# Kernel tuning notes

Hardware: AMD Instinct MI355X
Metric: run time of the kernel (lower is better)

## Reference

```python
import jax, jax.numpy as jnp
import numpy as np

H = 4  # head_num = 8 // 2
NEG = -1e9


def mha(x, mask, wqkv, bqkv, wo, bo):
    # x: [B, N, D], mask: [B, 1, N] (0 = masked key), wqkv: [3, D, D], wo: [D, Dout]
    B, N, D = x.shape
    dh = D // H
    q = (x @ wqkv[0] + bqkv[0]).reshape(B, N, H, dh)
    k = (x @ wqkv[1] + bqkv[1]).reshape(B, N, H, dh)
    v = (x @ wqkv[2] + bqkv[2]).reshape(B, N, H, dh)
    scores = jnp.einsum('bqhd,bkhd->bhqk', q, k) / jnp.sqrt(jnp.asarray(dh, x.dtype))
    scores = jnp.where(mask[:, None, :, :] == 0, NEG, scores)  # mask keys, bcast over heads/queries
    attn = jax.nn.softmax(scores, axis=-1)
    out = jnp.einsum('bhqk,bkhd->bqhd', attn, v).reshape(B, N, D)
    return out @ wo + bo


def setup_inputs() -> dict:
    key = jax.random.key(0)
    ks = jax.random.split(key, 24)
    B, M, F = 16, 32, 16
    N = M * M
    def w(k, shape, fan_in):
        return jax.random.normal(k, shape, dtype=jnp.float32) / np.sqrt(fan_in)
    return {
        'robot_1_node': jax.random.normal(ks[0], (B, M, F), dtype=jnp.float32),
        'robot_2_node': jax.random.normal(ks[1], (B, M, F), dtype=jnp.float32),
        'coop_edge_cost': jax.random.normal(ks[2], (B, M, M, F), dtype=jnp.float32),
        'coop_edge_mask': jax.random.randint(ks[3], (B, M, M), 0, 2, dtype=jnp.int32),
        'd1_wqkv': w(ks[4], (3, 48, 48), 48), 'd1_bqkv': jnp.zeros((3, 48), jnp.float32),
        'd1_wo': w(ks[5], (48, 16), 48), 'd1_bo': jnp.zeros((16,), jnp.float32),
        'd2_wqkv': w(ks[6], (3, 16, 16), 16), 'd2_bqkv': jnp.zeros((3, 16), jnp.float32),
        'd2_wo': w(ks[7], (16, 16), 16), 'd2_bo': jnp.zeros((16,), jnp.float32),
        'pol_wqkv': w(ks[8], (3, 16, 16), 16), 'pol_bqkv': jnp.zeros((3, 16), jnp.float32),
        'pol_wo': w(ks[9], (16, 1), 16), 'pol_bo': jnp.zeros((1,), jnp.float32),
        'val_wqkv': w(ks[10], (3, 16, 16), 16), 'val_bqkv': jnp.zeros((3, 16), jnp.float32),
        'val_wo': w(ks[11], (16, 1), 16), 'val_bo': jnp.zeros((1,), jnp.float32),
        'v2_w': w(ks[12], (N, 16), N), 'v2_b': jnp.zeros((16,), jnp.float32),
    }


def reference(robot_1_node, robot_2_node, coop_edge_cost, coop_edge_mask,
              d1_wqkv, d1_bqkv, d1_wo, d1_bo,
              d2_wqkv, d2_bqkv, d2_wo, d2_bo,
              pol_wqkv, pol_bqkv, pol_wo, pol_bo,
              val_wqkv, val_bqkv, val_wo, val_bo,
              v2_w, v2_b):
    B, M, F = robot_1_node.shape
    N = M * M
    edge = coop_edge_cost.reshape(B, N, -1)            # flatten(-3,-2)
    mask = coop_edge_mask.reshape(B, 1, N)             # flatten + unsqueeze(-2)
    f1 = jnp.broadcast_to(robot_1_node[:, :, None, :], (B, M, M, F)).reshape(B, N, F)
    f2 = jnp.broadcast_to(robot_2_node[:, None, :, :], (B, M, M, F)).reshape(B, N, F)
    f = jnp.concatenate([f1, f2, edge], axis=-1)       # [B, N, 3F]
    e = mha(f, mask, d1_wqkv, d1_bqkv, d1_wo, d1_bo)   # [B, N, 16]
    e = mha(e, mask, d2_wqkv, d2_bqkv, d2_wo, d2_bo)   # [B, N, 16]
    action = mha(e, mask, pol_wqkv, pol_bqkv, pol_wo, pol_bo).reshape(B, N)
    masked_action = jax.nn.softmax(jnp.where(mask[:, 0, :] == 0, NEG, action), axis=-1)
    critic = mha(e, mask, val_wqkv, val_bqkv, val_wo, val_bo).reshape(B, N)
    critic = critic @ v2_w + v2_b                       # [B, 16]
    return masked_action, critic
```

## Files before the change

kernel.cpp:

```cpp
#include <hip/hip_runtime.h>
#include <math.h>

#define NEGV (-1e9f)
#define LOG2E 1.4426950408889634f

typedef _Float16 f16;
typedef __attribute__((ext_vector_type(2))) __fp16 hf2;
typedef __attribute__((ext_vector_type(4))) _Float16 f16x4;
typedef __attribute__((ext_vector_type(4))) float f32x4;

__global__ void qkv1_prep_kernel(
    const float* __restrict__ r1, const float* __restrict__ r2,
    const float* __restrict__ edge,
    const float* __restrict__ d1_wqkv, const float* __restrict__ d1_bqkv,
    const float* __restrict__ d1_wo, const float* __restrict__ d1_bo,
    const float* __restrict__ d2_wqkv, const float* __restrict__ d2_bqkv,
    const float* __restrict__ d2_wo, const float* __restrict__ d2_bo,
    const float* __restrict__ pol_wqkv, const float* __restrict__ pol_bqkv,
    const float* __restrict__ val_wqkv, const float* __restrict__ val_bqkv,
    f16* __restrict__ q1h, f16* __restrict__ k1h, f16* __restrict__ v1h,
    float* __restrict__ Wf1, float* __restrict__ bf1,
    float* __restrict__ Wfp, float* __restrict__ bfp,
    float* __restrict__ Wfv, float* __restrict__ bfv,
    int B, int M, int F, int H, float qmul1, int mainBlocks) {
    const int N = M * M;
    const int BN = B * N;

    if ((int)blockIdx.x < mainBlocks) {
        int t = blockIdx.x * blockDim.x + threadIdx.x;
        if (t >= 3 * BN * 48) return;
        int col = t % 48;
        int row = (t / 48) % BN;
        int mat = t / (48 * BN);
        int b = row / N, n = row % N;
        int i = n / M, j = n % M;

        const float* f1 = r1 + (b * M + i) * F;
        const float* f2 = r2 + (b * M + j) * F;
        const float* fe = edge + (size_t)row * F;
        const float* w  = d1_wqkv + mat * 48 * 48 + col;

        float s = d1_bqkv[mat * 48 + col];
#pragma unroll
        for (int d = 0; d < 16; ++d) s = fmaf(f1[d], w[d * 48], s);
#pragma unroll
        for (int d = 0; d < 16; ++d) s = fmaf(f2[d], w[(16 + d) * 48], s);
#pragma unroll
        for (int d = 0; d < 16; ++d) s = fmaf(fe[d], w[(32 + d) * 48], s);

        int h = col / 12, dd = col % 12;
        size_t off = ((size_t)(b * H + h) * N + n) * 12 + dd;
        if (mat == 0)      q1h[off] = (f16)(s * qmul1);
        else if (mat == 1) k1h[off] = (f16)s;
        else               v1h[off] = (f16)s;
        return;
    }

    int t = (blockIdx.x - mainBlocks) * 256 + threadIdx.x;
    if (t < 2304) {
        int mat = t / 768, r = (t % 768) / 16, c = t % 16;
        float s = 0.f;
#pragma unroll
        for (int k = 0; k < 16; ++k)
            s = fmaf(d1_wo[r * 16 + k], d2_wqkv[mat * 256 + k * 16 + c], s);
        Wf1[t] = s;
        return;
    }
    int u = t - 2304;
    if (u < 48) {
        int mat = u / 16, c = u % 16;
        float s = d2_bqkv[mat * 16 + c];
#pragma unroll
        for (int k = 0; k < 16; ++k)
            s = fmaf(d1_bo[k], d2_wqkv[mat * 256 + k * 16 + c], s);
        bf1[u] = s;
        return;
    }
    u -= 48;
    if (u < 768) {
        int mat = u / 256, r = (u % 256) / 16, c = u % 16;
        float s = 0.f;
#pragma unroll
        for (int k = 0; k < 16; ++k)
            s = fmaf(d2_wo[r * 16 + k], pol_wqkv[mat * 256 + k * 16 + c], s);
        Wfp[u] = s;
        return;
    }
    u -= 768;
    if (u < 48) {
        int mat = u / 16, c = u % 16;
        float s = pol_bqkv[mat * 16 + c];
#pragma unroll
        for (int k = 0; k < 16; ++k)
            s = fmaf(d2_bo[k], pol_wqkv[mat * 256 + k * 16 + c], s);
        bfp[u] = s;
        return;
    }
    u -= 48;
    if (u < 768) {
        int mat = u / 256, r = (u % 256) / 16, c = u % 16;
        float s = 0.f;
#pragma unroll
        for (int k = 0; k < 16; ++k)
            s = fmaf(d2_wo[r * 16 + k], val_wqkv[mat * 256 + k * 16 + c], s);
        Wfv[u] = s;
        return;
    }
    u -= 768;
    if (u < 48) {
        int mat = u / 16, c = u % 16;
        float s = val_bqkv[mat * 16 + c];
#pragma unroll
        for (int k = 0; k < 16; ++k)
            s = fmaf(d2_bo[k], val_wqkv[mat * 256 + k * 16 + c], s);
        bfv[u] = s;
    }
}

template <int DH>
__device__ inline void attn_core(const f16* __restrict__ qh, const f16* __restrict__ kh,
                                 const f16* __restrict__ vh, const int* __restrict__ mask,
                                 int b, int qg, int H, int N,
                                 f16* __restrict__ Kt, f16* __restrict__ Vt,
                                 float* __restrict__ mbs,
                                 float* __restrict__ comb, int combStride) {
    int tid = threadIdx.x;
    int wave = tid >> 6, lane = tid & 63;
    int h = wave & 3, qhalf = wave >> 2;
    int lrow = lane & 15, lg = lane >> 4;
    int bhs = b * H + h;
    int qrow = qg * 32 + qhalf * 16 + lrow;

    f16x4 zf = {(f16)0.f, (f16)0.f, (f16)0.f, (f16)0.f};
    bool qok = (4 * lg < DH);
    f16x4 qf = qok ? *(const f16x4*)(qh + ((size_t)bhs * N + qrow) * DH + 4 * lg) : zf;

    f32x4 oacc = {0.f, 0.f, 0.f, 0.f};

    for (int chunk = 0; chunk < 4; ++chunk) {
        int kbase = chunk * 256;
        __syncthreads();
        for (int idx = tid; idx < 1024; idx += 512) {
            int hh = idx >> 8, kk = idx & 255;
            const f16* kB = kh + ((size_t)(b * H + hh) * N + kbase + kk) * DH;
            const f16* vB = vh + ((size_t)(b * H + hh) * N + kbase + kk) * DH;
#pragma unroll
            for (int d4 = 0; d4 < DH / 4; ++d4)
                ((uint2*)(Kt + ((size_t)hh * 256 + kk) * DH))[d4] = ((const uint2*)kB)[d4];
            uint2 vr[DH / 4];
#pragma unroll
            for (int d4 = 0; d4 < DH / 4; ++d4) vr[d4] = ((const uint2*)vB)[d4];
            const f16* vv = (const f16*)vr;
#pragma unroll
            for (int d = 0; d < DH; ++d)
                Vt[(hh * (DH + 1) + d) * 264 + kk] = vv[d];
            Vt[(hh * (DH + 1) + DH) * 264 + kk] = (f16)1.f;
        }
        if (tid < 256) mbs[tid] = mask[b * N + kbase + tid] ? (-8.f * LOG2E) : NEGV;
        __syncthreads();

        const f16* KtH = Kt + (size_t)h * 256 * DH;
        const f16* VtH = Vt + (size_t)h * (DH + 1) * 264;
#pragma unroll 8
        for (int t16 = 0; t16 < 16; ++t16) {
            f16x4 kf = *(const f16x4*)(KtH + (size_t)(t16 * 16 + lrow) * DH + 4 * lg);
            float4 mv = *(const float4*)(mbs + t16 * 16 + 4 * lg);
            f32x4 mc = {mv.x, mv.y, mv.z, mv.w};
            f16x4 vb = *(const f16x4*)(VtH + (size_t)lrow * 264 + t16 * 16 + 4 * lg);

            f32x4 s = __builtin_amdgcn_mfma_f32_16x16x16f16(kf, qf, mc, 0, 0, 0);
            hf2 lo = __builtin_amdgcn_cvt_pkrtz(__builtin_amdgcn_exp2f(s[0]),
                                                __builtin_amdgcn_exp2f(s[1]));
            hf2 hi = __builtin_amdgcn_cvt_pkrtz(__builtin_amdgcn_exp2f(s[2]),
                                                __builtin_amdgcn_exp2f(s[3]));
            f16x4 pa;
            ((hf2*)&pa)[0] = lo;
            ((hf2*)&pa)[1] = hi;
            oacc = __builtin_amdgcn_mfma_f32_16x16x16f16(pa, vb, oacc, 0, 0, 0);
        }
    }

    __syncthreads();
#pragma unroll
    for (int r = 0; r < 4; ++r) {
        float lr = __shfl(oacc[r], (lane & 48) | DH);
        if (lrow < DH)
            comb[(qhalf * 16 + lg * 4 + r) * combStride + h * DH + lrow] = oacc[r] / lr;
    }
    __syncthreads();
}

__global__ __launch_bounds__(512, 4) void attn1_fold1_kernel(
    const f16* __restrict__ q1h, const f16* __restrict__ k1h, const f16* __restrict__ v1h,
    const int* __restrict__ mask,
    const float* __restrict__ Wf1, const float* __restrict__ bf1,
    f16* __restrict__ q2h, f16* __restrict__ k2h, f16* __restrict__ v2h,
    int H, int N, float qmul2) {
    const int DH = 12;
    const int VROWS = 3 * (DH + 1) + 16;
    __shared__ __align__(16) f16 KtA[4 * 256 * DH];
    __shared__ __align__(16) f16 VtA[VROWS * 264];
    __shared__ __align__(16) float mbsA[256];

    int qg = blockIdx.x, b = blockIdx.y;
    float* comb = (float*)KtA;
    attn_core<DH>(q1h, k1h, v1h, mask, b, qg, H, N, KtA, VtA, mbsA, comb, 49);

    int tid = threadIdx.x;
#pragma unroll
    for (int k = 0; k < 3; ++k) {
        int idx = tid + k * 512;
        int mat = idx / 512, r = (idx % 512) / 16, c = idx % 16;
        float s = bf1[mat * 16 + c];
        const float* wcol = Wf1 + mat * 768 + c;
#pragma unroll
        for (int d = 0; d < 48; ++d)
            s = fmaf(comb[r * 49 + d], wcol[d * 16], s);
        int n = qg * 32 + r;
        int hh = c >> 2, dd = c & 3;
        size_t off = ((size_t)(b * H + hh) * N + n) * 4 + dd;
        if (mat == 0)      q2h[off] = (f16)(s * qmul2);
        else if (mat == 1) k2h[off] = (f16)s;
        else               v2h[off] = (f16)s;
    }
}

__global__ __launch_bounds__(512, 8) void attn2_fold2_kernel(
    const f16* __restrict__ q2h, const f16* __restrict__ k2h, const f16* __restrict__ v2h,
    const int* __restrict__ mask,
    const float* __restrict__ Wfp, const float* __restrict__ bfp,
    const float* __restrict__ Wfv, const float* __restrict__ bfv,
    f16* __restrict__ qph, f16* __restrict__ kph, f16* __restrict__ vph,
    f16* __restrict__ qvh, f16* __restrict__ kvh, f16* __restrict__ vvh,
    int H, int N, float qmul2) {
    const int DH = 4;
    const int VROWS = 3 * (DH + 1) + 16;
    __shared__ __align__(16) f16 KtA[4 * 256 * DH];
    __shared__ __align__(16) f16 VtA[VROWS * 264];
    __shared__ __align__(16) float mbsA[256];

    int qg = blockIdx.x, b = blockIdx.y;
    float* comb = (float*)KtA;
    attn_core<DH>(q2h, k2h, v2h, mask, b, qg, H, N, KtA, VtA, mbsA, comb, 17);

    int tid = threadIdx.x;
#pragma unroll
    for (int k = 0; k < 6; ++k) {
        int idx = tid + k * 512;
        int set = idx / 1536;
        int rem = idx % 1536;
        int mat = rem / 512, r = (rem % 512) / 16, c = rem % 16;
        const float* W  = set ? Wfv : Wfp;
        const float* bb = set ? bfv : bfp;
        float s = bb[mat * 16 + c];
        const float* wcol = W + mat * 256 + c;
#pragma unroll
        for (int d = 0; d < 16; ++d)
            s = fmaf(comb[r * 17 + d], wcol[d * 16], s);
        int n = qg * 32 + r;
        int hh = c >> 2, dd = c & 3;
        size_t off = ((size_t)(b * H + hh) * N + n) * 4 + dd;
        f16* dst;
        if (set == 0) dst = (mat == 0) ? qph : (mat == 1) ? kph : vph;
        else          dst = (mat == 0) ? qvh : (mat == 1) ? kvh : vvh;
        dst[off] = (f16)((mat == 0) ? s * qmul2 : s);
    }
}

__global__ __launch_bounds__(512, 8) void attn3_heads_kernel(
    const f16* __restrict__ qph, const f16* __restrict__ kph, const f16* __restrict__ vph,
    const f16* __restrict__ qvh, const f16* __restrict__ kvh, const f16* __restrict__ vvh,
    const int* __restrict__ mask,
    const float* __restrict__ pol_wo, const float* __restrict__ pol_bo,
    const float* __restrict__ val_wo, const float* __restrict__ val_bo,
    float* __restrict__ araw, float* __restrict__ craw,
    int H, int N) {
    const int DH = 4;
    const int VROWS = 3 * (DH + 1) + 16;
    __shared__ __align__(16) f16 KtA[4 * 256 * DH];
    __shared__ __align__(16) f16 VtA[VROWS * 264];
    __shared__ __align__(16) float mbsA[256];

    int qg = blockIdx.x, b = blockIdx.y, set = blockIdx.z;
    const f16* qh = set ? qvh : qph;
    const f16* kh = set ? kvh : kph;
    const f16* vh = set ? vvh : vph;
    float* comb = (float*)KtA;
    attn_core<DH>(qh, kh, vh, mask, b, qg, H, N, KtA, VtA, mbsA, comb, 17);

    int tid = threadIdx.x;
    if (tid < 32) {
        int r = tid;
        const float* wo = set ? val_wo : pol_wo;
        float s = (set ? val_bo : pol_bo)[0];
#pragma unroll
        for (int d = 0; d < 16; ++d) s = fmaf(comb[r * 17 + d], wo[d], s);
        (set ? craw : araw)[b * N + qg * 32 + r] = s;
    }
}

__global__ __launch_bounds__(256) void final_kernel(
    const float* __restrict__ araw, const int* __restrict__ mask,
    const float* __restrict__ craw, const float* __restrict__ v2w,
    const float* __restrict__ v2b,
    float* __restrict__ out_action, float* __restrict__ out_critic, int N, int B) {
    int tid = threadIdx.x;
    if ((int)blockIdx.x < B) {
        int b = blockIdx.x;
        int lane = tid & 63, wid = tid >> 6;
        __shared__ float wred[4];
        __shared__ float sbcast;

        float local[4];
        float mx = -INFINITY;
#pragma unroll
        for (int i = 0; i < 4; ++i) {
            int n = tid + i * 256;
            float a = araw[b * N + n];
            if (mask[b * N + n] == 0) a = NEGV;
            local[i] = a;
            mx = fmaxf(mx, a);
        }
#pragma unroll
        for (int o = 32; o > 0; o >>= 1) mx = fmaxf(mx, __shfl_down(mx, o));
        if (lane == 0) wred[wid] = mx;
        __syncthreads();
        if (tid == 0) sbcast = fmaxf(fmaxf(wred[0], wred[1]), fmaxf(wred[2], wred[3]));
        __syncthreads();
        mx = sbcast;

        float s = 0.f;
#pragma unroll
        for (int i = 0; i < 4; ++i) {
            float p = __expf(local[i] - mx);
            local[i] = p;
            s += p;
        }
#pragma unroll
        for (int o = 32; o > 0; o >>= 1) s += __shfl_down(s, o);
        if (lane == 0) wred[wid] = s;
        __syncthreads();
        if (tid == 0) sbcast = wred[0] + wred[1] + wred[2] + wred[3];
        __syncthreads();
        float inv = 1.f / sbcast;
#pragma unroll
        for (int i = 0; i < 4; ++i) out_action[b * N + tid + i * 256] = local[i] * inv;
    } else {
        int b = blockIdx.x - B;
        int c = tid & 15, seg = tid >> 4;
        __shared__ float red[16][17];
        float s = 0.f;
        int n0 = seg * 64;
        for (int n = n0; n < n0 + 64; ++n)
            s = fmaf(craw[b * N + n], v2w[n * 16 + c], s);
        red[seg][c] = s;
        __syncthreads();
        if (tid < 16) {
            float acc = v2b[tid];
#pragma unroll
            for (int g = 0; g < 16; ++g) acc += red[g][tid];
            out_critic[b * 16 + tid] = acc;
        }
    }
}

extern "C" void kernel_launch(void* const* d_in, const int* in_sizes, int n_in,
                              void* d_out, int out_size, void* d_ws, size_t ws_size,
                              hipStream_t stream) {
    const int B = 16, M = 32, F = 16, H = 4;
    const int N = M * M;
    const int BN = B * N;
    const int BHN = B * H * N;

    const float* r1       = (const float*)d_in[0];
    const float* r2       = (const float*)d_in[1];
    const float* edge     = (const float*)d_in[2];
    const int*   mask     = (const int*)d_in[3];
    const float* d1_wqkv  = (const float*)d_in[4];
    const float* d1_bqkv  = (const float*)d_in[5];
    const float* d1_wo    = (const float*)d_in[6];
    const float* d1_bo    = (const float*)d_in[7];
    const float* d2_wqkv  = (const float*)d_in[8];
    const float* d2_bqkv  = (const float*)d_in[9];
    const float* d2_wo    = (const float*)d_in[10];
    const float* d2_bo    = (const float*)d_in[11];
    const float* pol_wqkv = (const float*)d_in[12];
    const float* pol_bqkv = (const float*)d_in[13];
    const float* pol_wo   = (const float*)d_in[14];
    const float* pol_bo   = (const float*)d_in[15];
    const float* val_wqkv = (const float*)d_in[16];
    const float* val_bqkv = (const float*)d_in[17];
    const float* val_wo   = (const float*)d_in[18];
    const float* val_bo   = (const float*)d_in[19];
    const float* v2_w     = (const float*)d_in[20];
    const float* v2_b     = (const float*)d_in[21];

    float* ws = (float*)d_ws;
    float* Wf1  = ws;
    float* bf1  = Wf1 + 2304;
    float* Wfp  = bf1 + 48;
    float* bfp  = Wfp + 768;
    float* Wfv  = bfp + 48;
    float* bfv  = Wfv + 768;
    float* araw = bfv + 48;
    float* craw = araw + BN;
    f16* fh  = (f16*)(craw + BN);
    f16* q1h = fh;
    f16* k1h = q1h + (size_t)BHN * 12;
    f16* v1h = k1h + (size_t)BHN * 12;
    f16* q2h = v1h + (size_t)BHN * 12;
    f16* k2h = q2h + (size_t)BHN * 4;
    f16* v2h = k2h + (size_t)BHN * 4;
    f16* qph = v2h + (size_t)BHN * 4;
    f16* kph = qph + (size_t)BHN * 4;
    f16* vph = kph + (size_t)BHN * 4;
    f16* qvh = vph + (size_t)BHN * 4;
    f16* kvh = qvh + (size_t)BHN * 4;
    f16* vvh = kvh + (size_t)BHN * 4;

    float* out_action = (float*)d_out;
    float* out_critic = out_action + BN;

    const float qmul1 = (1.0f / sqrtf(12.0f)) * LOG2E;
    const float qmul2 = 0.5f * LOG2E;

    {
        int mainBlocks = (3 * BN * 48 + 255) / 256;
        qkv1_prep_kernel<<<mainBlocks + 16, 256, 0, stream>>>(
            r1, r2, edge, d1_wqkv, d1_bqkv, d1_wo, d1_bo,
            d2_wqkv, d2_bqkv, d2_wo, d2_bo,
            pol_wqkv, pol_bqkv, val_wqkv, val_bqkv,
            q1h, k1h, v1h, Wf1, bf1, Wfp, bfp, Wfv, bfv,
            B, M, F, H, qmul1, mainBlocks);
    }
    attn1_fold1_kernel<<<dim3(N / 32, B), 512, 0, stream>>>(
        q1h, k1h, v1h, mask, Wf1, bf1, q2h, k2h, v2h, H, N, qmul2);
    attn2_fold2_kernel<<<dim3(N / 32, B), 512, 0, stream>>>(
        q2h, k2h, v2h, mask, Wfp, bfp, Wfv, bfv,
        qph, kph, vph, qvh, kvh, vvh, H, N, qmul2);
    attn3_heads_kernel<<<dim3(N / 32, B, 2), 512, 0, stream>>>(
        qph, kph, vph, qvh, kvh, vvh, mask,
        pol_wo, pol_bo, val_wo, val_bo, araw, craw, H, N);
    final_kernel<<<2 * B, 256, 0, stream>>>(
        araw, mask, craw, v2_w, v2_b, out_action, out_critic, N, B);
}
```

Before: 107.3 us.

## Compute layer-1 QKV projection with MFMA tiles staged through shared memory

Replaces the one-thread-per-output scalar QKV projection with a tiled kernel. Each block stages 64 input rows (gathered from the two node arrays and the edge features) plus the full transposed weight set into LDS as fp16, then runs 16x16x16 f16 MFMA per wave. This removes the heavily redundant global loads and scalar FMAs of the previous version. In exchange, the projection inputs are now rounded to fp16 before the matmul, and N, M and H are hardcoded to the test shape.

Measured after the change: 97.76 us. 8.9% less time.

```diff
diff --git a/kernel.cpp b/kernel.cpp
--- a/kernel.cpp
+++ b/kernel.cpp
@@ -9,7 +9,7 @@
 typedef __attribute__((ext_vector_type(4))) _Float16 f16x4;
 typedef __attribute__((ext_vector_type(4))) float f32x4;
 
-__global__ void qkv1_prep_kernel(
+__global__ __launch_bounds__(256, 4) void qkv1_mfma_prep_kernel(
     const float* __restrict__ r1, const float* __restrict__ r2,
     const float* __restrict__ edge,
     const float* __restrict__ d1_wqkv, const float* __restrict__ d1_bqkv,
@@ -22,41 +22,67 @@
     float* __restrict__ Wf1, float* __restrict__ bf1,
     float* __restrict__ Wfp, float* __restrict__ bfp,
     float* __restrict__ Wfv, float* __restrict__ bfv,
-    int B, int M, int F, int H, float qmul1, int mainBlocks) {
-    const int N = M * M;
-    const int BN = B * N;
-
-    if ((int)blockIdx.x < mainBlocks) {
-        int t = blockIdx.x * blockDim.x + threadIdx.x;
-        if (t >= 3 * BN * 48) return;
-        int col = t % 48;
-        int row = (t / 48) % BN;
-        int mat = t / (48 * BN);
-        int b = row / N, n = row % N;
-        int i = n / M, j = n % M;
-
-        const float* f1 = r1 + (b * M + i) * F;
-        const float* f2 = r2 + (b * M + j) * F;
-        const float* fe = edge + (size_t)row * F;
-        const float* w  = d1_wqkv + mat * 48 * 48 + col;
-
-        float s = d1_bqkv[mat * 48 + col];
-#pragma unroll
-        for (int d = 0; d < 16; ++d) s = fmaf(f1[d], w[d * 48], s);
-#pragma unroll
-        for (int d = 0; d < 16; ++d) s = fmaf(f2[d], w[(16 + d) * 48], s);
-#pragma unroll
-        for (int d = 0; d < 16; ++d) s = fmaf(fe[d], w[(32 + d) * 48], s);
-
-        int h = col / 12, dd = col % 12;
-        size_t off = ((size_t)(b * H + h) * N + n) * 12 + dd;
-        if (mat == 0)      q1h[off] = (f16)(s * qmul1);
-        else if (mat == 1) k1h[off] = (f16)s;
-        else               v1h[off] = (f16)s;
-        return;
-    }
-
-    int t = (blockIdx.x - mainBlocks) * 256 + threadIdx.x;
+    float qmul1) {
+    const int N = 1024, M = 32, H = 4;
+
+    if ((int)blockIdx.x < 256) {
+        __shared__ __align__(16) f16 Ft[64 * 50];
+        __shared__ __align__(16) f16 Wt[144 * 50];
+        int tid = threadIdx.x;
+        int row0 = blockIdx.x * 64;
+        int b = row0 / N;
+
+        for (int idx = tid; idx < 64 * 48; idx += 256) {
+            int rr = idx / 48, c = idx % 48;
+            int n = (row0 + rr) % N;
+            int i = n / M, j = n % M;
+            float v;
+            if (c < 16)      v = r1[(b * M + i) * 16 + c];
+            else if (c < 32) v = r2[(b * M + j) * 16 + (c - 16)];
+            else             v = edge[(size_t)(row0 + rr) * 16 + (c - 32)];
+            Ft[rr * 50 + c] = (f16)v;
+        }
+        for (int idx = tid; idx < 6912; idx += 256) {
+            int mat = idx / 2304, rem = idx % 2304;
+            int k = rem / 48, c = rem % 48;
+            Wt[(mat * 48 + c) * 50 + k] = (f16)d1_wqkv[mat * 2304 + k * 48 + c];
+        }
+        __syncthreads();
+
+        int lane = tid & 63, wave = tid >> 6;
+        int lrow = lane & 15, lg = lane >> 4;
+
+        const f16* Frow = Ft + (wave * 16 + lrow) * 50;
+        f16x4 af[3];
+#pragma unroll
+        for (int kt = 0; kt < 3; ++kt)
+            af[kt] = *(const f16x4*)(Frow + kt * 16 + 4 * lg);
+
+#pragma unroll
+        for (int ct = 0; ct < 9; ++ct) {
+            int gcol = ct * 16 + lrow;
+            int mat = gcol / 48, c48 = gcol % 48;
+            float bias = d1_bqkv[mat * 48 + c48];
+            f32x4 acc = {bias, bias, bias, bias};
+            const f16* Wcol = Wt + gcol * 50;
+#pragma unroll
+            for (int kt = 0; kt < 3; ++kt) {
+                f16x4 bf = *(const f16x4*)(Wcol + kt * 16 + 4 * lg);
+                acc = __builtin_amdgcn_mfma_f32_16x16x16f16(af[kt], bf, acc, 0, 0, 0);
+            }
+            int h = c48 / 12, dd = c48 % 12;
+            f16* dst = (mat == 0) ? q1h : (mat == 1) ? k1h : v1h;
+            float mul = (mat == 0) ? qmul1 : 1.f;
+#pragma unroll
+            for (int r = 0; r < 4; ++r) {
+                int n = (row0 + wave * 16 + 4 * lg + r) % N;
+                dst[((size_t)(b * H + h) * N + n) * 12 + dd] = (f16)(acc[r] * mul);
+            }
+        }
+        return;
+    }
+
+    int t = (blockIdx.x - 256) * 256 + threadIdx.x;
     if (t < 2304) {
         int mat = t / 768, r = (t % 768) / 16, c = t % 16;
         float s = 0.f;
@@ -424,15 +450,11 @@
     const float qmul1 = (1.0f / sqrtf(12.0f)) * LOG2E;
     const float qmul2 = 0.5f * LOG2E;
 
-    {
-        int mainBlocks = (3 * BN * 48 + 255) / 256;
-        qkv1_prep_kernel<<<mainBlocks + 16, 256, 0, stream>>>(
-            r1, r2, edge, d1_wqkv, d1_bqkv, d1_wo, d1_bo,
-            d2_wqkv, d2_bqkv, d2_wo, d2_bo,
-            pol_wqkv, pol_bqkv, val_wqkv, val_bqkv,
-            q1h, k1h, v1h, Wf1, bf1, Wfp, bfp, Wfv, bfv,
-            B, M, F, H, qmul1, mainBlocks);
-    }
+    qkv1_mfma_prep_kernel<<<256 + 16, 256, 0, stream>>>(
+        r1, r2, edge, d1_wqkv, d1_bqkv, d1_wo, d1_bo,
+        d2_wqkv, d2_bqkv, d2_wo, d2_bo,
+        pol_wqkv, pol_bqkv, val_wqkv, val_bqkv,
+        q1h, k1h, v1h, Wf1, bf1, Wfp, bfp, Wfv, bfv, qmul1);
     attn1_fold1_kernel<<<dim3(N / 32, B), 512, 0, stream>>>(
         q1h, k1h, v1h, mask, Wf1, bf1, q2h, k2h, v2h, H, N, qmul2);
     attn2_fold2_kernel<<<dim3(N / 32, B), 512, 0, stream>>>(
```
